# Performance work log

Measured on AMD Instinct MI355X. Metric: run time of the kernel, lower is better.

The kernel has to match this reference:

```python
import jax, jax.numpy as jnp
import numpy as np

B, T, D = 2, 4096, 1024
HD, HQ, KVH, W = 128, 8, 1, 1024   # head_dim, q_heads, kv_heads, window
HH, HG, K = 1536, 2048, 4          # hawk hidden, gmlp hidden, conv kernel
ALPHA_SCALE = float(np.log(8.0))   # alpha_log_scale (stored as log, used exp'd)


def setup_inputs() -> dict:
    key = jax.random.key(0)
    ks = jax.random.split(key, 16)
    n = lambda k, shape, std: jax.random.normal(k, shape, jnp.float32) * std
    return {
        'x': n(ks[0], (B, T, D), 1.0),
        'sn_g': jnp.ones((D,), jnp.float32),
        'q_w': n(ks[1], (HQ * HD, D), D ** -0.5),
        'kv_w': n(ks[2], (2 * KVH * HD, D), D ** -0.5),
        'ao_w': n(ks[3], (D, D), D ** -0.5),
        'sgn_g': jnp.ones((D,), jnp.float32),
        'sg_grow': n(ks[4], (2 * HG, D), D ** -0.5),
        'sg_shrink': n(ks[5], (D, HG), HG ** -0.5),
        'hn_g': jnp.ones((D,), jnp.float32),
        'h_in_w': n(ks[6], (2 * HH, D), D ** -0.5),
        'h_conv_w': n(ks[7], (HH, 1, K), K ** -0.5),
        'h_conv_b': jnp.zeros((HH,), jnp.float32),
        'h_gates_w': n(ks[8], (2 * HH, HH), HH ** -0.5),
        'h_gates_b': jnp.zeros((2 * HH,), jnp.float32),
        'h_forget': jnp.linspace(-4.323, -9.0, HH, dtype=jnp.float32),
        'h_out_w': n(ks[9], (D, HH), HH ** -0.5),
        'hgn_g': jnp.ones((D,), jnp.float32),
        'hg_grow': n(ks[10], (2 * HG, D), D ** -0.5),
        'hg_shrink': n(ks[11], (D, HG), HG ** -0.5),
    }


def rmsnorm(x, gamma):
    # original: gamma / dim**-0.5 * x / ||x||_2  (no eps)
    inv = jax.lax.rsqrt(jnp.sum(x * x, axis=-1, keepdims=True))
    return gamma * (x.shape[-1] ** 0.5) * x * inv


def rope(x, base=10000.0):
    # x: (B, T, H, HD); interleaved rotary over time axis 1
    t = x.shape[1]
    hd = x.shape[-1]
    inv = 1.0 / (base ** (jnp.arange(0, hd, 2, dtype=jnp.float32) / hd))
    ang = jnp.arange(t, dtype=jnp.float32)[:, None] * inv[None, :]  # (T, HD/2)
    cos = jnp.cos(ang)[None, :, None, :]
    sin = jnp.sin(ang)[None, :, None, :]
    x1, x2 = x[..., 0::2], x[..., 1::2]
    y1 = x1 * cos - x2 * sin
    y2 = x1 * sin + x2 * cos
    return jnp.stack([y1, y2], axis=-1).reshape(x.shape)


def sliding_mqa(x, q_w, kv_w, ao_w):
    # MQA with causal sliding window of W, computed in blocks of W
    q = (x @ q_w.T).reshape(B, T, HQ, HD)
    kv = (x @ kv_w.T).reshape(B, T, 2, KVH, HD)
    k = kv[:, :, 0, 0]  # (B, T, HD) since KVH == 1
    v = kv[:, :, 1, 0]
    q = rope(q)
    k = rope(k[:, :, None, :])[:, :, 0]
    nb = T // W
    qb = q.reshape(B, nb, W, HQ, HD)
    kb = k.reshape(B, nb, W, HD)
    vb = v.reshape(B, nb, W, HD)
    # prepend previous block (zeros for block 0)
    shift = lambda a: jnp.concatenate([jnp.zeros_like(a[:, :1]), a[:, :-1]], axis=1)
    k2 = jnp.concatenate([shift(kb), kb], axis=2)  # (B, nb, 2W, HD)
    v2 = jnp.concatenate([shift(vb), vb], axis=2)
    qi = jnp.arange(W)[:, None]
    kj = jnp.arange(2 * W)[None, :]
    base = (kj >= qi) & (kj <= qi + W)  # causal + window (i-j <= W)
    blk0 = base & (kj >= W)             # block 0 has no real previous block
    mask = jnp.where(jnp.arange(nb)[:, None, None] == 0, blk0[None], base[None])
    scores = jnp.einsum('bnqhd,bnkd->bhnqk', qb, k2) * (HD ** -0.5)
    scores = jnp.where(mask[None, None], scores, -jnp.inf)
    p = jax.nn.softmax(scores, axis=-1)
    o = jnp.einsum('bhnqk,bnkd->bnqhd', p, v2).reshape(B, T, HQ * HD)
    return o @ ao_w.T


def gated_mlp(x, grow_w, shrink_w):
    gate, h = jnp.split(x @ grow_w.T, 2, axis=-1)
    return (jax.nn.gelu(gate, approximate=False) * h) @ shrink_w.T


def hawk(x, in_w, conv_w, conv_b, gates_w, gates_b, forget_base, out_w):
    gate, u = jnp.split(x @ in_w.T, 2, axis=-1)  # (B, T, HH) each
    # depthwise causal conv1d (torch pads k-1 both sides then slices [:T])
    u_nch = jnp.transpose(u, (0, 2, 1))  # (B, HH, T)
    c = jax.lax.conv_general_dilated(
        u_nch, conv_w, window_strides=(1,), padding=[(K - 1, 0)],
        feature_group_count=HH, dimension_numbers=('NCH', 'OIH', 'NCH'))
    xc = jnp.transpose(c + conv_b[None, :, None], (0, 2, 1))  # (B, T, HH)
    fg, ig = jnp.split(xc @ gates_w.T + gates_b, 2, axis=-1)
    log_alpha = -np.exp(ALPHA_SCALE) * jax.nn.softplus(forget_base) * jax.nn.sigmoid(fg)
    alpha = jnp.exp(log_alpha)
    beta = jnp.sqrt(1.0 - alpha * alpha + 1e-6)
    xin = beta * jax.nn.sigmoid(ig) * xc
    # linear recurrence h_t = alpha_t * h_{t-1} + xin_t  via associative scan
    def combine(c1, c2):
        a1, x1 = c1
        a2, x2 = c2
        return a1 * a2, a2 * x1 + x2
    _, h = jax.lax.associative_scan(combine, (alpha, xin), axis=1)
    return (jax.nn.gelu(gate, approximate=False) * h) @ out_w.T


def reference(x, sn_g, q_w, kv_w, ao_w, sgn_g, sg_grow, sg_shrink,
              hn_g, h_in_w, h_conv_w, h_conv_b, h_gates_w, h_gates_b,
              h_forget, h_out_w, hgn_g, hg_grow, hg_shrink):
    x = x + sliding_mqa(rmsnorm(x, sn_g), q_w, kv_w, ao_w)
    x = x + gated_mlp(rmsnorm(x, sgn_g), sg_grow, sg_shrink)
    x = x + hawk(rmsnorm(x, hn_g), h_in_w, h_conv_w, h_conv_b,
                 h_gates_w, h_gates_b, h_forget, h_out_w)
    x = x + gated_mlp(rmsnorm(x, hgn_g), hg_grow, hg_shrink)
    return x
```

## Files before the change

kernel.cpp:

```cpp
#include <hip/hip_runtime.h>
#include <hip/hip_bf16.h>
#include <math.h>

#define B_  2
#define T_  4096
#define D_  1024
#define HD_ 128
#define HQ_ 8
#define W_  1024
#define HH_ 1536
#define HG_ 2048
#define KC_ 4

typedef float  f32x4  __attribute__((ext_vector_type(4)));
typedef float  f32x2  __attribute__((ext_vector_type(2)));
typedef __bf16 bf16x8 __attribute__((ext_vector_type(8)));
typedef unsigned short u16;
typedef unsigned short u16x2 __attribute__((ext_vector_type(2)));
typedef unsigned short u16x4 __attribute__((ext_vector_type(4)));
typedef unsigned short u16x8 __attribute__((ext_vector_type(8)));

__device__ __forceinline__ u16 f2bf(float f) {
    unsigned int u = __builtin_bit_cast(unsigned int, f);
    u += 0x7fffu + ((u >> 16) & 1u);
    return (u16)(u >> 16);
}
__device__ __forceinline__ float bf2f(u16 v) {
    unsigned int u = ((unsigned int)v) << 16;
    return __builtin_bit_cast(float, u);
}
__device__ __forceinline__ float gelu_exact(float x) {
    return 0.5f * x * (1.0f + erff(x * 0.70710678118654752f));
}
__device__ __forceinline__ float sigmoidf_(float x) {
    return 1.0f / (1.0f + expf(-x));
}

#define GLOAD16(gp, lp) __builtin_amdgcn_global_load_lds( \
    (const __attribute__((address_space(1))) void*)(gp),  \
    (__attribute__((address_space(3))) void*)(lp), 16, 0, 0)

struct CvtArgs {
    const float* src[10];
    u16* dst[10];
    long cum[11];
};
__global__ __launch_bounds__(256)
void cvt_all_kernel(CvtArgs a)
{
    long i = ((long)blockIdx.x * 256 + threadIdx.x) * 8;
    if (i >= a.cum[10]) return;
    int seg = 0;
#pragma unroll
    for (int s = 1; s < 10; s++) if (i >= a.cum[s]) seg = s;
    long off = i - a.cum[seg];
    const float* src = a.src[seg];
    u16* dst = a.dst[seg];
    f32x4 x = *(const f32x4*)(src + off);
    f32x4 y = *(const f32x4*)(src + off + 4);
    u16x4 ua, ub;
    ua.x = f2bf(x.x); ua.y = f2bf(x.y); ua.z = f2bf(x.z); ua.w = f2bf(x.w);
    ub.x = f2bf(y.x); ub.y = f2bf(y.y); ub.z = f2bf(y.z); ub.w = f2bf(y.w);
    *(u16x4*)(dst + off) = ua;
    *(u16x4*)(dst + off + 4) = ub;
}

template<int EPI, bool OBF>
__global__ __launch_bounds__(512)
void gemm_big_kernel(const u16* __restrict__ A, const u16* __restrict__ Bw,
                     const float* __restrict__ bias, const float* __restrict__ res,
                     const u16* gatebuf, void* outv,
                     int M, int N, int K)
{
    __shared__ u16 lA[3][256 * 32];
    __shared__ u16 lB[3][128 * 32];
    const int n0 = blockIdx.x * 128, m0 = blockIdx.y * 256;
    const int tid = threadIdx.x, w = tid >> 6, l = tid & 63;
    const int wr = w >> 1, wc = w & 1;
    const int lr = l & 15, lg = l >> 4;

    f32x4 acc[4][4];
#pragma unroll
    for (int i = 0; i < 4; i++)
#pragma unroll
        for (int j = 0; j < 4; j++) acc[i][j] = {0.f, 0.f, 0.f, 0.f};

    const int srow = tid >> 2;
    const int gslot = (((tid) & 3) - ((tid >> 3) & 3)) & 3;
    const u16* gA = A + (long)(m0 + srow) * K + gslot * 8;
    const u16* gB = Bw + (long)(n0 + srow) * K + gslot * 8;
    const int lofs = tid * 8;

#define STAGE_G(buf, kk)                                            \
    {                                                               \
        GLOAD16(gA + (kk),                 &lA[buf][lofs]);         \
        GLOAD16(gA + (long)128 * K + (kk), &lA[buf][4096 + lofs]);  \
        GLOAD16(gB + (kk),                 &lB[buf][lofs]);         \
    }

    const int NT = K >> 5;
    STAGE_G(0, 0);
    STAGE_G(1, 32);

    const int swzr = (lr >> 1) & 3;
    int cur = 0;
    for (int t = 0; t < NT; ++t) {
        if (t == NT - 1) { asm volatile("s_waitcnt vmcnt(0)" ::: "memory"); }
        else             { asm volatile("s_waitcnt vmcnt(3)" ::: "memory"); }
        __builtin_amdgcn_s_barrier();
        __builtin_amdgcn_sched_barrier(0);
        if (t + 2 < NT) {
            int nb = cur + 2; if (nb >= 3) nb -= 3;
            STAGE_G(nb, (t + 2) << 5);
        }
        bf16x8 af[4], bfr[4];
#pragma unroll
        for (int m = 0; m < 4; m++)
            af[m] = *(const bf16x8*)&lA[cur][(wr * 64 + m * 16 + lr) * 32 + (((lg + swzr) & 3) * 8)];
#pragma unroll
        for (int n = 0; n < 4; n++)
            bfr[n] = *(const bf16x8*)&lB[cur][(wc * 64 + n * 16 + lr) * 32 + (((lg + swzr) & 3) * 8)];
        __builtin_amdgcn_s_setprio(1);
#pragma unroll
        for (int m = 0; m < 4; m++)
#pragma unroll
            for (int n = 0; n < 4; n++)
                acc[m][n] = __builtin_amdgcn_mfma_f32_16x16x32_bf16(af[m], bfr[n], acc[m][n], 0, 0, 0);
        __builtin_amdgcn_s_setprio(0);
        cur++; if (cur == 3) cur = 0;
    }
#undef STAGE_G

#pragma unroll
    for (int m = 0; m < 4; m++)
#pragma unroll
        for (int n = 0; n < 4; n++) {
            const int col = n0 + wc * 64 + n * 16 + lr;
            const float bv = (EPI == 1) ? bias[col] : 0.f;
#pragma unroll
            for (int r = 0; r < 4; r++) {
                const int row = m0 + wr * 64 + m * 16 + lg * 4 + r;
                const long idx = (long)row * N + col;
                float v = acc[m][n][r] + bv;
                if (EPI == 2) v += res[idx];
                if (EPI == 3) v = gelu_exact(bf2f(gatebuf[idx])) * v;
                if (OBF) ((u16*)outv)[idx] = f2bf(v);
                else     ((float*)outv)[idx] = v;
            }
        }
}

template<int EPI, bool OBF>
__global__ __launch_bounds__(256)
void gemm_bf16_kernel(const u16* __restrict__ A, const u16* __restrict__ Bw,
                      const float* __restrict__ bias, const float* __restrict__ res,
                      const u16* gatebuf, void* outv,
                      int M, int N, int K)
{
    __shared__ u16 lA[3][128 * 32];
    __shared__ u16 lB[3][128 * 32];
    const int n0 = blockIdx.x * 128, m0 = blockIdx.y * 128;
    const int tid = threadIdx.x, w = tid >> 6, l = tid & 63;
    const int wr = w >> 1, wc = w & 1, lr = l & 15, lg = l >> 4;

    f32x4 acc[4][4];
#pragma unroll
    for (int i = 0; i < 4; i++)
#pragma unroll
        for (int j = 0; j < 4; j++) acc[i][j] = {0.f, 0.f, 0.f, 0.f};

    const int srow = w * 16 + (l >> 2);
    const int gslot = ((l & 3) - ((l >> 3) & 3)) & 3;
    const u16* gA = A + (long)(m0 + srow) * K + gslot * 8;
    const u16* gB = Bw + (long)(n0 + srow) * K + gslot * 8;
    const int lofs = w * 512 + l * 8;

#define STAGE_G(buf, kk)                                          \
    {                                                             \
        GLOAD16(gA + (kk),                &lA[buf][lofs]);        \
        GLOAD16(gA + (long)64 * K + (kk), &lA[buf][2048 + lofs]); \
        GLOAD16(gB + (kk),                &lB[buf][lofs]);        \
        GLOAD16(gB + (long)64 * K + (kk), &lB[buf][2048 + lofs]); \
    }

    const int NT = K >> 5;
    STAGE_G(0, 0);
    STAGE_G(1, 32);

    const int swzr = (lr >> 1) & 3;
    int cur = 0;
    for (int t = 0; t < NT; ++t) {
        if (t == NT - 1) { asm volatile("s_waitcnt vmcnt(0)" ::: "memory"); }
        else             { asm volatile("s_waitcnt vmcnt(4)" ::: "memory"); }
        __builtin_amdgcn_s_barrier();
        __builtin_amdgcn_sched_barrier(0);
        if (t + 2 < NT) {
            int nb = cur + 2; if (nb >= 3) nb -= 3;
            STAGE_G(nb, (t + 2) << 5);
        }
        bf16x8 af[4], bfr[4];
#pragma unroll
        for (int m = 0; m < 4; m++)
            af[m] = *(const bf16x8*)&lA[cur][(wr * 64 + m * 16 + lr) * 32 + (((lg + swzr) & 3) * 8)];
#pragma unroll
        for (int n = 0; n < 4; n++)
            bfr[n] = *(const bf16x8*)&lB[cur][(wc * 64 + n * 16 + lr) * 32 + (((lg + swzr) & 3) * 8)];
        __builtin_amdgcn_s_setprio(1);
#pragma unroll
        for (int m = 0; m < 4; m++)
#pragma unroll
            for (int n = 0; n < 4; n++)
                acc[m][n] = __builtin_amdgcn_mfma_f32_16x16x32_bf16(af[m], bfr[n], acc[m][n], 0, 0, 0);
        __builtin_amdgcn_s_setprio(0);
        cur++; if (cur == 3) cur = 0;
    }
#undef STAGE_G

#pragma unroll
    for (int m = 0; m < 4; m++)
#pragma unroll
        for (int n = 0; n < 4; n++) {
            const int col = n0 + wc * 64 + n * 16 + lr;
            const float bv = (EPI == 1) ? bias[col] : 0.f;
#pragma unroll
            for (int r = 0; r < 4; r++) {
                const int row = m0 + wr * 64 + m * 16 + lg * 4 + r;
                const long idx = (long)row * N + col;
                float v = acc[m][n][r] + bv;
                if (EPI == 2) v += res[idx];
                if (EPI == 3) v = gelu_exact(bf2f(gatebuf[idx])) * v;
                if (OBF) ((u16*)outv)[idx] = f2bf(v);
                else     ((float*)outv)[idx] = v;
            }
        }
}

__global__ __launch_bounds__(256)
void rmsnorm_kernel(const float* __restrict__ x, const float* __restrict__ g,
                    u16* __restrict__ out)
{
    const long row = blockIdx.x;
    const int tid = threadIdx.x;
    const float* xp = x + row * D_;
    f32x4 v = *(const f32x4*)(xp + tid * 4);
    float ss = v.x * v.x + v.y * v.y + v.z * v.z + v.w * v.w;
#pragma unroll
    for (int o = 1; o < 64; o <<= 1) ss += __shfl_xor(ss, o);
    __shared__ float ps[4];
    if ((tid & 63) == 0) ps[tid >> 6] = ss;
    __syncthreads();
    float tot = ps[0] + ps[1] + ps[2] + ps[3];
    float inv = rsqrtf(tot) * 32.0f;
    f32x4 gv = *(const f32x4*)(g + tid * 4);
    u16x4 o4;
    o4.x = f2bf(gv.x * v.x * inv); o4.y = f2bf(gv.y * v.y * inv);
    o4.z = f2bf(gv.z * v.z * inv); o4.w = f2bf(gv.w * v.w * inv);
    *(u16x4*)(out + row * D_ + tid * 4) = o4;
}

__global__ void rope_bf16_kernel(const float* __restrict__ q, const float* __restrict__ kv,
                                 u16* __restrict__ qb, u16* __restrict__ kb)
{
    const long NQ = (long)B_ * T_ * HQ_ * 64;
    const long NK = (long)B_ * T_ * 64;
    long idx = (long)blockIdx.x * blockDim.x + threadIdx.x;
    if (idx >= NQ + NK) return;
    int i; long t; const float* src; u16* dst;
    if (idx < NQ) {
        i = idx & 63;
        long bth = idx >> 6;
        t = (bth / HQ_) % T_;
        src = q + bth * HD_ + 2 * i;
        dst = qb + bth * HD_ + 2 * i;
    } else {
        long k = idx - NQ;
        i = k & 63;
        long bt = k >> 6;
        t = bt % T_;
        src = kv + bt * (2 * HD_) + 2 * i;
        dst = kb + bt * HD_ + 2 * i;
    }
    float freq = exp2f(-(float)i * 0.20762050593046014f);
    float ang = (float)t * freq;
    float sn, cs;
    sincosf(ang, &sn, &cs);
    f32x2 xv = *(const f32x2*)src;
    u16x2 yv;
    yv.x = f2bf(xv.x * cs - xv.y * sn);
    yv.y = f2bf(xv.x * sn + xv.y * cs);
    *(u16x2*)dst = yv;
}

__global__ __launch_bounds__(256)
void vtrans_kernel(const float* __restrict__ kv, u16* __restrict__ vt)
{
    __shared__ float tile[64][65];
    const int t0 = blockIdx.x * 64, d0 = blockIdx.y * 64, b = blockIdx.z;
    const int tid = threadIdx.x;
    {
        const int tl = tid & 63, dg = tid >> 6;
        const float* vp = kv + (((long)b * T_ + t0 + tl) * 2 + 1) * HD_ + d0 + dg * 16;
#pragma unroll
        for (int j = 0; j < 4; j++) {
            f32x4 v = *(const f32x4*)(vp + j * 4);
            tile[dg * 16 + j * 4 + 0][tl] = v.x;
            tile[dg * 16 + j * 4 + 1][tl] = v.y;
            tile[dg * 16 + j * 4 + 2][tl] = v.z;
            tile[dg * 16 + j * 4 + 3][tl] = v.w;
        }
    }
    __syncthreads();
    {
        const int dl = tid >> 2, tg = (tid & 3) * 16;
        u16x8 a, c;
#pragma unroll
        for (int j = 0; j < 8; j++) a[j] = f2bf(tile[dl][tg + j]);
#pragma unroll
        for (int j = 0; j < 8; j++) c[j] = f2bf(tile[dl][tg + 8 + j]);
        u16* dst = vt + ((long)b * HD_ + d0 + dl) * T_ + t0 + tg;
        *(u16x8*)dst = a;
        *(u16x8*)(dst + 8) = c;
    }
}

#define PLD 72

__global__ __launch_bounds__(256)
void attn_mfma3_kernel(const u16* __restrict__ qb, const u16* __restrict__ kb,
                       const u16* __restrict__ vt, u16* __restrict__ o)
{
    __shared__ u16 Ksh[2][64 * 128];
    __shared__ u16 Vsh[2][128 * 64];
    __shared__ u16 Psh[4 * 16 * PLD];

    const int qt = blockIdx.x, h = blockIdx.y, b = blockIdx.z;
    const int q0 = qt * 64;
    const int tid = threadIdx.x;
    const int w = tid >> 6, l = tid & 63;
    const int lr = l & 15, lg = l >> 4;

    bf16x8 qfr[4];
    {
        const u16* qp = qb + (((long)b * T_ + q0 + w * 16 + lr) * HQ_ + h) * HD_;
#pragma unroll
        for (int kt = 0; kt < 4; kt++)
            qfr[kt] = *(const bf16x8*)(qp + kt * 32 + lg * 8);
    }

    int oK[4], oV[4];
#pragma unroll
    for (int i = 0; i < 4; i++) {
        int krow = w * 16 + i * 4 + (l >> 4);
        int kc8 = (l & 15) ^ (krow & 7);
        oK[i] = krow * 128 + kc8 * 8;
        int vrow = w * 32 + i * 8 + (l >> 3);
        int vc8 = (l & 7) ^ (vrow & 7);
        oV[i] = vrow * T_ + vc8 * 8;
    }
    const u16* kbase = kb + (long)b * T_ * HD_;
    const u16* vbase = vt + (long)b * HD_ * T_;

    f32x4 oacc[8];
#pragma unroll
    for (int dt = 0; dt < 8; dt++) oacc[dt] = {0.f, 0.f, 0.f, 0.f};
    float mrun[4], srun[4];
#pragma unroll
    for (int r = 0; r < 4; r++) { mrun[r] = -1e30f; srun[r] = 0.f; }

    const int kt_lo = (q0 >= W_) ? (q0 - W_) : 0;
    const int nt = ((q0 - kt_lo) >> 6) + 1;
    const int sw = lr & 7;
    const float scale = 0.08838834764831845f;

#pragma unroll
    for (int i = 0; i < 4; i++) {
        GLOAD16(kbase + (long)kt_lo * HD_ + oK[i], &Ksh[0][w * 2048 + i * 512]);
        GLOAD16(vbase + kt_lo + oV[i], &Vsh[0][w * 2048 + i * 512]);
    }

    for (int t = 0; t < nt; ++t) {
        const int kt0 = kt_lo + t * 64;
        const int cur = t & 1;
        if (t + 1 < nt) {
            const int ktn = kt0 + 64;
#pragma unroll
            for (int i = 0; i < 4; i++) {
                GLOAD16(kbase + (long)ktn * HD_ + oK[i], &Ksh[cur ^ 1][w * 2048 + i * 512]);
                GLOAD16(vbase + ktn + oV[i], &Vsh[cur ^ 1][w * 2048 + i * 512]);
            }
            asm volatile("s_waitcnt vmcnt(8)" ::: "memory");
        } else {
            asm volatile("s_waitcnt vmcnt(0)" ::: "memory");
        }
        __builtin_amdgcn_s_barrier();
        __builtin_amdgcn_sched_barrier(0);

        const u16* Kc = Ksh[cur];
        const u16* Vc = Vsh[cur];

        f32x4 s[4];
        __builtin_amdgcn_s_setprio(1);
#pragma unroll
        for (int ct = 0; ct < 4; ct++) {
            s[ct] = {0.f, 0.f, 0.f, 0.f};
#pragma unroll
            for (int kt = 0; kt < 4; kt++) {
                bf16x8 kf = *(const bf16x8*)&Kc[(ct * 16 + lr) * 128 + (((kt * 4 + lg) ^ sw) * 8)];
                s[ct] = __builtin_amdgcn_mfma_f32_16x16x32_bf16(qfr[kt], kf, s[ct], 0, 0, 0);
            }
        }
        __builtin_amdgcn_s_setprio(0);

        float tmax[4] = {-3e38f, -3e38f, -3e38f, -3e38f};
        if (kt0 == q0) {
#pragma unroll
            for (int ct = 0; ct < 4; ct++) {
                const int kpos = kt0 + ct * 16 + lr;
#pragma unroll
                for (int r = 0; r < 4; r++) {
                    const int qpos = q0 + w * 16 + lg * 4 + r;
                    float v = s[ct][r] * scale;
                    v = (kpos <= qpos) ? v : -3e38f;
                    s[ct][r] = v;
                    tmax[r] = fmaxf(tmax[r], v);
                }
            }
        } else if (kt0 == q0 - W_) {
#pragma unroll
            for (int ct = 0; ct < 4; ct++) {
                const int kpos = kt0 + ct * 16 + lr;
#pragma unroll
                for (int r = 0; r < 4; r++) {
                    const int qpos = q0 + w * 16 + lg * 4 + r;
                    float v = s[ct][r] * scale;
                    v = (kpos + W_ >= qpos) ? v : -3e38f;
                    s[ct][r] = v;
                    tmax[r] = fmaxf(tmax[r], v);
                }
            }
        } else {
#pragma unroll
            for (int ct = 0; ct < 4; ct++)
#pragma unroll
                for (int r = 0; r < 4; r++) {
                    float v = s[ct][r] * scale;
                    s[ct][r] = v;
                    tmax[r] = fmaxf(tmax[r], v);
                }
        }
#pragma unroll
        for (int r = 0; r < 4; r++)
#pragma unroll
            for (int msk = 1; msk < 16; msk <<= 1)
                tmax[r] = fmaxf(tmax[r], __shfl_xor(tmax[r], msk));

        bool defer = (tmax[0] <= mrun[0] + 8.f) && (tmax[1] <= mrun[1] + 8.f) &&
                     (tmax[2] <= mrun[2] + 8.f) && (tmax[3] <= mrun[3] + 8.f);
        if (!__all(defer)) {
            float frv[4];
#pragma unroll
            for (int r = 0; r < 4; r++) {
                float mnew = fmaxf(mrun[r], tmax[r]);
                frv[r] = __expf(mrun[r] - mnew);
                mrun[r] = mnew;
                srun[r] *= frv[r];
            }
#pragma unroll
            for (int dt = 0; dt < 8; dt++) {
                oacc[dt][0] *= frv[0]; oacc[dt][1] *= frv[1];
                oacc[dt][2] *= frv[2]; oacc[dt][3] *= frv[3];
            }
        }

        u16* pw = &Psh[w * 16 * PLD];
        float psum[4] = {0.f, 0.f, 0.f, 0.f};
#pragma unroll
        for (int ct = 0; ct < 4; ct++)
#pragma unroll
            for (int r = 0; r < 4; r++) {
                float p = __expf(s[ct][r] - mrun[r]);
                psum[r] += p;
                pw[(lg * 4 + r) * PLD + ct * 16 + lr] = f2bf(p);
            }
#pragma unroll
        for (int r = 0; r < 4; r++) {
#pragma unroll
            for (int msk = 1; msk < 16; msk <<= 1)
                psum[r] += __shfl_xor(psum[r], msk);
            srun[r] += psum[r];
        }

        asm volatile("s_waitcnt lgkmcnt(0)" ::: "memory");
        bf16x8 pa0 = *(const bf16x8*)&pw[lr * PLD + lg * 8];
        bf16x8 pa1 = *(const bf16x8*)&pw[lr * PLD + 32 + lg * 8];
        __builtin_amdgcn_s_setprio(1);
#pragma unroll
        for (int dt = 0; dt < 8; dt++) {
            bf16x8 vf0 = *(const bf16x8*)&Vc[(dt * 16 + lr) * 64 + ((lg ^ sw) * 8)];
            bf16x8 vf1 = *(const bf16x8*)&Vc[(dt * 16 + lr) * 64 + (((4 + lg) ^ sw) * 8)];
            oacc[dt] = __builtin_amdgcn_mfma_f32_16x16x32_bf16(pa0, vf0, oacc[dt], 0, 0, 0);
            oacc[dt] = __builtin_amdgcn_mfma_f32_16x16x32_bf16(pa1, vf1, oacc[dt], 0, 0, 0);
        }
        __builtin_amdgcn_s_setprio(0);
        __syncthreads();
    }

#pragma unroll
    for (int r = 0; r < 4; r++) {
        const int qpos = q0 + w * 16 + lg * 4 + r;
        float inv = 1.f / srun[r];
        u16* op = o + ((long)b * T_ + qpos) * (HQ_ * HD_) + h * HD_;
#pragma unroll
        for (int dt = 0; dt < 8; dt++)
            op[dt * 16 + lr] = f2bf(oacc[dt][r] * inv);
    }
}

__global__ void conv_kernel(const u16* __restrict__ u, const float* __restrict__ w,
                            const float* __restrict__ bias, u16* __restrict__ xc)
{
    long idx = (long)blockIdx.x * blockDim.x + threadIdx.x;
    if (idx >= (long)B_ * T_ * HH_) return;
    int ch = (int)(idx % HH_);
    long row = idx / HH_;
    int t = (int)(row % T_);
    float acc = bias[ch];
#pragma unroll
    for (int k = 0; k < KC_; k++) {
        int ts = t - 3 + k;
        if (ts >= 0) acc += bf2f(u[(row - t + ts) * HH_ + ch]) * w[ch * KC_ + k];
    }
    xc[idx] = f2bf(acc);
}

#define CS_ 64
#define NC_ (T_ / CS_)

__device__ __forceinline__ void alpha_xin(const u16 fg, const u16 ig, const u16 xc,
                                          float sp, float& a, float& xin)
{
    a = expf(-8.0f * sp * sigmoidf_(bf2f(fg)));
    xin = sqrtf(1.f - a * a + 1e-6f) * sigmoidf_(bf2f(ig)) * bf2f(xc);
}

__global__ void scan1_kernel(const u16* __restrict__ fg, const u16* __restrict__ ig,
                             const u16* __restrict__ xc, const float* __restrict__ fb,
                             float* __restrict__ P, float* __restrict__ L)
{
    long idx = (long)blockIdx.x * blockDim.x + threadIdx.x;
    if (idx >= (long)B_ * NC_ * HH_) return;
    int ch = (int)(idx % HH_);
    int chunk = (int)((idx / HH_) % NC_);
    int b = (int)(idx / ((long)HH_ * NC_));
    long base = ((long)b * T_ + chunk * CS_) * HH_ + ch;
    float f = fb[ch];
    float sp = (f > 20.f) ? f : log1pf(expf(f));
    float p = 1.f, lacc = 0.f;
    for (int i = 0; i < CS_; i++) {
        long o = base + (long)i * HH_;
        float a, xin;
        alpha_xin(fg[o], ig[o], xc[o], sp, a, xin);
        lacc = a * lacc + xin;
        p *= a;
    }
    P[idx] = p; L[idx] = lacc;
}
__global__ void scan2_kernel(const float* __restrict__ P, const float* __restrict__ L,
                             float* __restrict__ I)
{
    long idx = (long)blockIdx.x * blockDim.x + threadIdx.x;
    if (idx >= (long)B_ * HH_) return;
    int ch = (int)(idx % HH_);
    int b = (int)(idx / HH_);
    float init = 0.f;
    for (int c = 0; c < NC_; c++) {
        long o = ((long)b * NC_ + c) * HH_ + ch;
        I[o] = init;
        init = P[o] * init + L[o];
    }
}
__global__ void scan3_kernel(const u16* __restrict__ fg, const u16* __restrict__ ig,
                             const u16* __restrict__ xc, const float* __restrict__ fb,
                             const float* __restrict__ I, const u16* __restrict__ gate,
                             u16* __restrict__ glu)
{
    long idx = (long)blockIdx.x * blockDim.x + threadIdx.x;
    if (idx >= (long)B_ * NC_ * HH_) return;
    int ch = (int)(idx % HH_);
    int chunk = (int)((idx / HH_) % NC_);
    int b = (int)(idx / ((long)HH_ * NC_));
    long base = ((long)b * T_ + chunk * CS_) * HH_ + ch;
    float f = fb[ch];
    float sp = (f > 20.f) ? f : log1pf(expf(f));
    float h = I[idx];
    for (int i = 0; i < CS_; i++) {
        long o = base + (long)i * HH_;
        float a, xin;
        alpha_xin(fg[o], ig[o], xc[o], sp, a, xin);
        h = a * h + xin;
        glu[o] = f2bf(gelu_exact(bf2f(gate[o])) * h);
    }
}

static inline long cdivl(long a, long b) { return (a + b - 1) / b; }

extern "C" void kernel_launch(void* const* d_in, const int* in_sizes, int n_in,
                              void* d_out, int out_size, void* d_ws, size_t ws_size,
                              hipStream_t stream)
{
    const float* x_in   = (const float*)d_in[0];
    const float* sn_g   = (const float*)d_in[1];
    const float* q_w    = (const float*)d_in[2];
    const float* kv_w   = (const float*)d_in[3];
    const float* ao_w   = (const float*)d_in[4];
    const float* sgn_g  = (const float*)d_in[5];
    const float* sg_grow   = (const float*)d_in[6];
    const float* sg_shrink = (const float*)d_in[7];
    const float* hn_g   = (const float*)d_in[8];
    const float* h_in_w = (const float*)d_in[9];
    const float* h_conv_w = (const float*)d_in[10];
    const float* h_conv_b = (const float*)d_in[11];
    const float* h_gates_w = (const float*)d_in[12];
    const float* h_gates_b = (const float*)d_in[13];
    const float* h_forget  = (const float*)d_in[14];
    const float* h_out_w   = (const float*)d_in[15];
    const float* hgn_g  = (const float*)d_in[16];
    const float* hg_grow   = (const float*)d_in[17];
    const float* hg_shrink = (const float*)d_in[18];
    float* out = (float*)d_out;

    char* wsb = (char*)d_ws;
    u16* Wq  = (u16*)wsb;
    u16* Wkv = Wq  + 1048576;
    u16* Wao = Wkv + 262144;
    u16* Wsg = Wao + 1048576;
    u16* Wss = Wsg + 4194304;
    u16* Whi = Wss + 2097152;
    u16* Whg = Whi + 3145728;
    u16* Who = Whg + 4718592;
    u16* Wgg = Who + 1572864;
    u16* Wgs = Wgg + 4194304;
    char* ab = wsb + 48758784;
    u16*   XN   = (u16*)(ab + 0);
    char*  S2   = ab + 16777216;
    char*  S3   = ab + 50331648;
    char*  S4   = ab + 75497472;
    char*  S5   = ab + 100663296;
    char*  S6   = ab + 125829120;
    float* PB   = (float*)(ab + 150994944);
    float* LB   = (float*)(ab + 151781376);
    float* IB   = (float*)(ab + 152567808);

    const long M = (long)B_ * T_;
    dim3 blk(256);
    dim3 blk5(512);
    const float* NULF = nullptr;
    const u16*   NULB = nullptr;

    {
        CvtArgs ca;
        const float* srcs[10] = {q_w, kv_w, ao_w, sg_grow, sg_shrink,
                                 h_in_w, h_gates_w, h_out_w, hg_grow, hg_shrink};
        u16* dsts[10] = {Wq, Wkv, Wao, Wsg, Wss, Whi, Whg, Who, Wgg, Wgs};
        long ns[10] = {1048576, 262144, 1048576, 4194304, 2097152,
                       3145728, 4718592, 1572864, 4194304, 2097152};
        long cum = 0;
        for (int i = 0; i < 10; i++) {
            ca.src[i] = srcs[i]; ca.dst[i] = dsts[i]; ca.cum[i] = cum; cum += ns[i];
        }
        ca.cum[10] = cum;
        cvt_all_kernel<<<dim3(cdivl(cum / 8, 256)), blk, 0, stream>>>(ca);
    }

    {
        float* Q  = (float*)S2;
        float* KV = (float*)S3;
        u16*   Kb = (u16*)(S3 + 8388608);
        u16*   Vt = (u16*)(S3 + 10485760);
        u16*   Qb = (u16*)S4;
        u16*   AT = (u16*)S5;
        rmsnorm_kernel<<<dim3(M), blk, 0, stream>>>(x_in, sn_g, XN);
        gemm_big_kernel<0,false><<<dim3(8, 32), blk5, 0, stream>>>(XN, Wq, NULF, NULF, NULB, Q, M, 1024, 1024);
        gemm_bf16_kernel<0,false><<<dim3(2, 64), blk, 0, stream>>>(XN, Wkv, NULF, NULF, NULB, KV, M, 256, 1024);
        rope_bf16_kernel<<<dim3(cdivl((long)B_ * T_ * (HQ_ + 1) * 64, 256)), blk, 0, stream>>>(Q, KV, Qb, Kb);
        vtrans_kernel<<<dim3(T_ / 64, 2, B_), blk, 0, stream>>>(KV, Vt);
        attn_mfma3_kernel<<<dim3(T_ / 64, HQ_, B_), blk, 0, stream>>>(Qb, Kb, Vt, AT);
        gemm_big_kernel<2,false><<<dim3(8, 32), blk5, 0, stream>>>(AT, Wao, NULF, x_in, NULB, out, M, 1024, 1024);
    }

    {
        u16* GATE = (u16*)S2;
        rmsnorm_kernel<<<dim3(M), blk, 0, stream>>>(out, sgn_g, XN);
        gemm_big_kernel<0,true><<<dim3(16, 32), blk5, 0, stream>>>(XN, Wsg, NULF, NULF, NULB, GATE, M, 2048, 1024);
        gemm_big_kernel<3,true><<<dim3(16, 32), blk5, 0, stream>>>(XN, Wsg + (size_t)2048 * 1024, NULF, NULF, GATE, GATE, M, 2048, 1024);
        gemm_big_kernel<2,false><<<dim3(8, 32), blk5, 0, stream>>>(GATE, Wss, NULF, out, NULB, out, M, 1024, 2048);
    }

    {
        u16* GATEH = (u16*)S2;
        u16* U     = (u16*)S3;
        u16* XC    = (u16*)S4;
        u16* FG    = (u16*)S5;
        u16* IG    = (u16*)S6;
        rmsnorm_kernel<<<dim3(M), blk, 0, stream>>>(out, hn_g, XN);
        gemm_big_kernel<0,true><<<dim3(12, 32), blk5, 0, stream>>>(XN, Whi, NULF, NULF, NULB, GATEH, M, 1536, 1024);
        gemm_big_kernel<0,true><<<dim3(12, 32), blk5, 0, stream>>>(XN, Whi + (size_t)1536 * 1024, NULF, NULF, NULB, U, M, 1536, 1024);
        conv_kernel<<<dim3(cdivl(M * HH_, 256)), blk, 0, stream>>>(U, h_conv_w, h_conv_b, XC);
        gemm_big_kernel<1,true><<<dim3(12, 32), blk5, 0, stream>>>(XC, Whg, h_gates_b, NULF, NULB, FG, M, 1536, 1536);
        gemm_big_kernel<1,true><<<dim3(12, 32), blk5, 0, stream>>>(XC, Whg + (size_t)1536 * 1536, h_gates_b + 1536, NULF, NULB, IG, M, 1536, 1536);
        scan1_kernel<<<dim3(cdivl((long)B_ * NC_ * HH_, 256)), blk, 0, stream>>>(FG, IG, XC, h_forget, PB, LB);
        scan2_kernel<<<dim3(cdivl((long)B_ * HH_, 256)), blk, 0, stream>>>(PB, LB, IB);
        scan3_kernel<<<dim3(cdivl((long)B_ * NC_ * HH_, 256)), blk, 0, stream>>>(FG, IG, XC, h_forget, IB, GATEH, U);
        gemm_big_kernel<2,false><<<dim3(8, 32), blk5, 0, stream>>>(U, Who, NULF, out, NULB, out, M, 1024, 1536);
    }

    {
        u16* GLU = (u16*)S2;
        rmsnorm_kernel<<<dim3(M), blk, 0, stream>>>(out, hgn_g, XN);
        gemm_big_kernel<0,true><<<dim3(16, 32), blk5, 0, stream>>>(XN, Wgg, NULF, NULF, NULB, GLU, M, 2048, 1024);
        gemm_big_kernel<3,true><<<dim3(16, 32), blk5, 0, stream>>>(XN, Wgg + (size_t)2048 * 1024, NULF, NULF, GLU, GLU, M, 2048, 1024);
        gemm_big_kernel<2,false><<<dim3(8, 32), blk5, 0, stream>>>(GLU, Wgs, NULF, out, NULB, out, M, 1024, 2048);
    }
}
```

Before: 1.049 ms.

## Read attention K/V directly from global memory and use smaller GEMMs for Hawk

```diff
diff --git a/kernel.cpp b/kernel.cpp
--- a/kernel.cpp
+++ b/kernel.cpp
@@ -326,11 +326,9 @@
 #define PLD 72
 
 __global__ __launch_bounds__(256)
-void attn_mfma3_kernel(const u16* __restrict__ qb, const u16* __restrict__ kb,
+void attn_mfma4_kernel(const u16* __restrict__ qb, const u16* __restrict__ kb,
                        const u16* __restrict__ vt, u16* __restrict__ o)
 {
-    __shared__ u16 Ksh[2][64 * 128];
-    __shared__ u16 Vsh[2][128 * 64];
     __shared__ u16 Psh[4 * 16 * PLD];
 
     const int qt = blockIdx.x, h = blockIdx.y, b = blockIdx.z;
@@ -347,16 +345,6 @@
             qfr[kt] = *(const bf16x8*)(qp + kt * 32 + lg * 8);
     }
 
-    int oK[4], oV[4];
-#pragma unroll
-    for (int i = 0; i < 4; i++) {
-        int krow = w * 16 + i * 4 + (l >> 4);
-        int kc8 = (l & 15) ^ (krow & 7);
-        oK[i] = krow * 128 + kc8 * 8;
-        int vrow = w * 32 + i * 8 + (l >> 3);
-        int vc8 = (l & 7) ^ (vrow & 7);
-        oV[i] = vrow * T_ + vc8 * 8;
-    }
     const u16* kbase = kb + (long)b * T_ * HD_;
     const u16* vbase = vt + (long)b * HD_ * T_;
 
@@ -369,47 +357,21 @@
 
     const int kt_lo = (q0 >= W_) ? (q0 - W_) : 0;
     const int nt = ((q0 - kt_lo) >> 6) + 1;
-    const int sw = lr & 7;
     const float scale = 0.08838834764831845f;
-
-#pragma unroll
-    for (int i = 0; i < 4; i++) {
-        GLOAD16(kbase + (long)kt_lo * HD_ + oK[i], &Ksh[0][w * 2048 + i * 512]);
-        GLOAD16(vbase + kt_lo + oV[i], &Vsh[0][w * 2048 + i * 512]);
-    }
 
     for (int t = 0; t < nt; ++t) {
         const int kt0 = kt_lo + t * 64;
-        const int cur = t & 1;
-        if (t + 1 < nt) {
-            const int ktn = kt0 + 64;
-#pragma unroll
-            for (int i = 0; i < 4; i++) {
-                GLOAD16(kbase + (long)ktn * HD_ + oK[i], &Ksh[cur ^ 1][w * 2048 + i * 512]);
-                GLOAD16(vbase + ktn + oV[i], &Vsh[cur ^ 1][w * 2048 + i * 512]);
-            }
-            asm volatile("s_waitcnt vmcnt(8)" ::: "memory");
-        } else {
-            asm volatile("s_waitcnt vmcnt(0)" ::: "memory");
-        }
-        __builtin_amdgcn_s_barrier();
-        __builtin_amdgcn_sched_barrier(0);
-
-        const u16* Kc = Ksh[cur];
-        const u16* Vc = Vsh[cur];
 
         f32x4 s[4];
-        __builtin_amdgcn_s_setprio(1);
 #pragma unroll
         for (int ct = 0; ct < 4; ct++) {
             s[ct] = {0.f, 0.f, 0.f, 0.f};
 #pragma unroll
             for (int kt = 0; kt < 4; kt++) {
-                bf16x8 kf = *(const bf16x8*)&Kc[(ct * 16 + lr) * 128 + (((kt * 4 + lg) ^ sw) * 8)];
+                bf16x8 kf = *(const bf16x8*)&kbase[(kt0 + ct * 16 + lr) * HD_ + kt * 32 + lg * 8];
                 s[ct] = __builtin_amdgcn_mfma_f32_16x16x32_bf16(qfr[kt], kf, s[ct], 0, 0, 0);
             }
         }
-        __builtin_amdgcn_s_setprio(0);
 
         float tmax[4] = {-3e38f, -3e38f, -3e38f, -3e38f};
         if (kt0 == q0) {
@@ -496,13 +458,12 @@
         __builtin_amdgcn_s_setprio(1);
 #pragma unroll
         for (int dt = 0; dt < 8; dt++) {
-            bf16x8 vf0 = *(const bf16x8*)&Vc[(dt * 16 + lr) * 64 + ((lg ^ sw) * 8)];
-            bf16x8 vf1 = *(const bf16x8*)&Vc[(dt * 16 + lr) * 64 + (((4 + lg) ^ sw) * 8)];
+            bf16x8 vf0 = *(const bf16x8*)&vbase[(dt * 16 + lr) * T_ + kt0 + lg * 8];
+            bf16x8 vf1 = *(const bf16x8*)&vbase[(dt * 16 + lr) * T_ + kt0 + 32 + lg * 8];
             oacc[dt] = __builtin_amdgcn_mfma_f32_16x16x32_bf16(pa0, vf0, oacc[dt], 0, 0, 0);
             oacc[dt] = __builtin_amdgcn_mfma_f32_16x16x32_bf16(pa1, vf1, oacc[dt], 0, 0, 0);
         }
         __builtin_amdgcn_s_setprio(0);
-        __syncthreads();
     }
 
 #pragma unroll
@@ -684,7 +645,7 @@
         gemm_bf16_kernel<0,false><<<dim3(2, 64), blk, 0, stream>>>(XN, Wkv, NULF, NULF, NULB, KV, M, 256, 1024);
         rope_bf16_kernel<<<dim3(cdivl((long)B_ * T_ * (HQ_ + 1) * 64, 256)), blk, 0, stream>>>(Q, KV, Qb, Kb);
         vtrans_kernel<<<dim3(T_ / 64, 2, B_), blk, 0, stream>>>(KV, Vt);
-        attn_mfma3_kernel<<<dim3(T_ / 64, HQ_, B_), blk, 0, stream>>>(Qb, Kb, Vt, AT);
+        attn_mfma4_kernel<<<dim3(T_ / 64, HQ_, B_), blk, 0, stream>>>(Qb, Kb, Vt, AT);
         gemm_big_kernel<2,false><<<dim3(8, 32), blk5, 0, stream>>>(AT, Wao, NULF, x_in, NULB, out, M, 1024, 1024);
     }
 
@@ -703,11 +664,11 @@
         u16* FG    = (u16*)S5;
         u16* IG    = (u16*)S6;
         rmsnorm_kernel<<<dim3(M), blk, 0, stream>>>(out, hn_g, XN);
-        gemm_big_kernel<0,true><<<dim3(12, 32), blk5, 0, stream>>>(XN, Whi, NULF, NULF, NULB, GATEH, M, 1536, 1024);
-        gemm_big_kernel<0,true><<<dim3(12, 32), blk5, 0, stream>>>(XN, Whi + (size_t)1536 * 1024, NULF, NULF, NULB, U, M, 1536, 1024);
+        gemm_bf16_kernel<0,true><<<dim3(12, 64), blk, 0, stream>>>(XN, Whi, NULF, NULF, NULB, GATEH, M, 1536, 1024);
+        gemm_bf16_kernel<0,true><<<dim3(12, 64), blk, 0, stream>>>(XN, Whi + (size_t)1536 * 1024, NULF, NULF, NULB, U, M, 1536, 1024);
         conv_kernel<<<dim3(cdivl(M * HH_, 256)), blk, 0, stream>>>(U, h_conv_w, h_conv_b, XC);
-        gemm_big_kernel<1,true><<<dim3(12, 32), blk5, 0, stream>>>(XC, Whg, h_gates_b, NULF, NULB, FG, M, 1536, 1536);
-        gemm_big_kernel<1,true><<<dim3(12, 32), blk5, 0, stream>>>(XC, Whg + (size_t)1536 * 1536, h_gates_b + 1536, NULF, NULB, IG, M, 1536, 1536);
+        gemm_bf16_kernel<1,true><<<dim3(12, 64), blk, 0, stream>>>(XC, Whg, h_gates_b, NULF, NULB, FG, M, 1536, 1536);
+        gemm_bf16_kernel<1,true><<<dim3(12, 64), blk, 0, stream>>>(XC, Whg + (size_t)1536 * 1536, h_gates_b + 1536, NULF, NULB, IG, M, 1536, 1536);
         scan1_kernel<<<dim3(cdivl((long)B_ * NC_ * HH_, 256)), blk, 0, stream>>>(FG, IG, XC, h_forget, PB, LB);
         scan2_kernel<<<dim3(cdivl((long)B_ * HH_, 256)), blk, 0, stream>>>(PB, LB, IB);
         scan3_kernel<<<dim3(cdivl((long)B_ * NC_ * HH_, 256)), blk, 0, stream>>>(FG, IG, XC, h_forget, IB, GATEH, U);
```

Measured after the change: 1.235 ms. 1.18x slower.
